# Optimization experiments

Measured on AMD Instinct MI355X. Metric: run time of the kernel, lower is better.

The kernel has to match this reference:

```python
import jax, jax.numpy as jnp
import numpy as np
from jax import lax

STRIDE = 16
RATIOS = (0.5, 1.0, 2.0)
SCALES = (128.0, 256.0, 512.0)


def _anchor_template():
    # template[i] = [stride/2, stride/2, w, h], i = ri*3 + si
    r = jnp.asarray(RATIOS, jnp.float32)[:, None]        # (3,1)
    s = jnp.asarray(SCALES, jnp.float32)[None, :]        # (1,3)
    sqrt_r = jnp.sqrt(r)
    w = (s / sqrt_r)                                     # (3,3)
    h = (s * sqrt_r)
    half = jnp.full_like(w, STRIDE / 2.0)
    return jnp.stack([half, half, w, h], axis=-1).reshape(9, 4)  # (9,4) xywh


def setup_inputs() -> dict:
    key = jax.random.key(0)
    ks = jax.random.split(key, 6)
    B, C, H, W = 8, 512, 50, 76
    feature_maps = jax.random.normal(ks[0], (B, C, H, W), jnp.float32)
    conv_w = jax.random.normal(ks[1], (512, 512, 3, 3), jnp.float32) * 0.01
    conv_b = jnp.zeros((512,), jnp.float32)
    cls_w = jax.random.normal(ks[2], (18, 512, 1, 1), jnp.float32) * 0.01
    cls_b = jnp.zeros((18,), jnp.float32)
    reg_w = jax.random.normal(ks[3], (36, 512, 1, 1), jnp.float32) * 0.01
    reg_b = jnp.zeros((36,), jnp.float32)
    # (width, height) per image; x is clamped to im_size[0], y to im_size[1]
    img_size = jnp.tile(jnp.array([[W * STRIDE, H * STRIDE]], jnp.int32), (B, 1))
    return {"feature_maps": feature_maps, "conv_w": conv_w, "conv_b": conv_b,
            "cls_w": cls_w, "cls_b": cls_b, "reg_w": reg_w, "reg_b": reg_b,
            "img_size": img_size}


def reference(feature_maps, conv_w, conv_b, cls_w, cls_b, reg_w, reg_b, img_size):
    B, C, H, W = feature_maps.shape
    # 3x3 conv, pad=1, stride=1 + ReLU
    f = lax.conv_general_dilated(feature_maps, conv_w, (1, 1), 'SAME',
                                 dimension_numbers=('NCHW', 'OIHW', 'NCHW'))
    f = jax.nn.relu(f + conv_b[None, :, None, None])
    # 1x1 heads, then NCHW -> BHWC (matches the two torch transposes)
    cls = jnp.einsum('bchw,oc->bhwo', f, cls_w.reshape(18, 512)) + cls_b
    reg = jnp.einsum('bchw,oc->bhwo', f, reg_w.reshape(36, 512)) + reg_b
    cls = cls.reshape(B, H, W, 9, 2)
    reg = reg.reshape(B, H, W, 9, 4)

    # Vectorized anchor generation (replaces nested hi/wi loops)
    tmpl = _anchor_template()                              # (9,4)
    sx = (jnp.arange(W, dtype=jnp.float32) * STRIDE)[None, :]   # (1,W)
    sy = (jnp.arange(H, dtype=jnp.float32) * STRIDE)[:, None]   # (H,1)
    zeros = jnp.zeros((H, W), jnp.float32)
    shift = jnp.stack([jnp.broadcast_to(sx, (H, W)),
                       jnp.broadcast_to(sy, (H, W)), zeros, zeros], axis=-1)  # (H,W,4)
    anchors = tmpl[None, None] + shift[:, :, None, :]      # (H,W,9,4)
    anchors = jnp.broadcast_to(anchors, (B, H, W, 9, 4)).reshape(B, -1, 4)

    cls = cls.reshape(B, -1, 2)
    reg = reg.reshape(B, -1, 4)

    # anchor2bbox: inverse of the target encoding in loss()
    axy, awh = anchors[..., :2], anchors[..., 2:]
    pxy = axy + reg[..., :2] * awh
    pwh = awh * jnp.exp(reg[..., 2:])

    # eval-mode clip to image bounds (vectorized over batch)
    im = img_size.astype(jnp.float32)[:, None, :]          # (B,1,2) = (w,h)
    x1y1 = pxy - pwh / 2
    x2y2 = x1y1 + pwh
    x1y1 = jnp.clip(x1y1, 0.0, im)
    x2y2 = jnp.clip(x2y2, 0.0, im)
    wh = x2y2 - x1y1
    cxy = x1y1 + wh / 2
    proposals = jnp.concatenate([cxy, wh], axis=-1)        # (B, H*W*9, 4)
    return (proposals, cls)
```

## Files before the change

### kernel.cpp

```cpp
#include <hip/hip_runtime.h>

typedef __attribute__((ext_vector_type(8))) __bf16 bf16x8;
typedef __attribute__((ext_vector_type(4))) float  f32x4;

#define GPTR(p)   (__attribute__((address_space(1))) void*)(p)
#define LDSPTR(p) (__attribute__((address_space(3))) void*)(p)
#define MFMA16 __builtin_amdgcn_mfma_f32_16x16x32_bf16
#define SB() __builtin_amdgcn_sched_barrier(0)

__device__ __forceinline__ unsigned short f2bf(float f) {
    union { float f; unsigned u; } v; v.f = f;
    unsigned r = v.u + 0x7FFF + ((v.u >> 16) & 1);
    return (unsigned short)(r >> 16);
}

#define MTOT   30400
#define MPAD   30464
#define KTOT   4608
#define NT     72

__global__ __launch_bounds__(256) void prep_all(
    const float* __restrict__ cw,
    const float* __restrict__ cls_w, const float* __restrict__ reg_w,
    const float* __restrict__ cls_b, const float* __restrict__ reg_b,
    const float* __restrict__ fm,
    unsigned short* __restrict__ Wt,
    unsigned short* __restrict__ W2, float* __restrict__ b2,
    unsigned short* __restrict__ P)
{
    __shared__ float t[32][65];
    int bid = blockIdx.x;
    if (bid < 9216) {
        int i = bid * 256 + threadIdx.x;
        int o = i / KTOT;
        int r = i - o * KTOT;
        int kk = r >> 9;
        int c  = r & 511;
        Wt[i] = f2bf(cw[(o * 512 + c) * 9 + kk]);
    } else if (bid < 9344) {
        int i = (bid - 9216) * 256 + threadIdx.x;
        int n = i >> 9, k = i & 511;
        float v = 0.f;
        if (n < 18) v = cls_w[n * 512 + k];
        else if (n < 54) v = reg_w[(n - 18) * 512 + k];
        W2[i] = f2bf(v);
        if (i < 64) {
            float bv = 0.f;
            if (i < 18) bv = cls_b[i];
            else if (i < 54) bv = reg_b[i - 18];
            b2[i] = bv;
        }
    } else if (bid < 9856) {
        int i = (bid - 9344) * 256 + threadIdx.x;
        int b   = i >> 14;
        int rem = i & 16383;
        int seg = rem >> 6;
        int c8  = (rem & 63) << 3;
        int y, x;
        if (seg < 78)       { y = 0;  x = seg; }
        else if (seg < 156) { y = 51; x = seg - 78; }
        else if (seg < 206) { y = seg - 155; x = 0; }
        else                { y = seg - 205; x = 77; }
        *(float4*)(P + ((b * 52 + y) * 78 + x) * 512 + c8) = make_float4(0.f, 0.f, 0.f, 0.f);
    } else {
        int bid2 = bid - 9856;
        const int tid = threadIdx.x;
        const int tx  = tid & 31;
        const int ty  = tid >> 5;
        const int xp  = bid2 % 24;
        const int tix = xp % 3;
        const int cix = xp / 3;
        const int y   = (bid2 / 24) % 50;
        const int b   = bid2 / 1200;
        const int x0  = tix * 32, c0 = cix * 64;

        const int x = x0 + tx;
        if (x < 76) {
#pragma unroll
            for (int i = 0; i < 8; ++i) {
                int cc = i * 8 + ty;
                t[tx][cc] = fm[((b * 512 + c0 + cc) * 50 + y) * 76 + x];
            }
        }
        __syncthreads();

        const int p = tid >> 6;
        const int c = tid & 63;
#pragma unroll
        for (int xi = 0; xi < 8; ++xi) {
            int xr = p * 8 + xi;
            int xw = x0 + xr;
            if (xw < 76)
                P[((b * 52 + y + 1) * 78 + (xw + 1)) * 512 + c0 + c] = f2bf(t[xr][c]);
        }
    }
}

__global__ __launch_bounds__(512, 2) void conv_gemm8(
    const unsigned short* __restrict__ P,
    const unsigned short* __restrict__ Wt,
    const float* __restrict__ bias,
    unsigned short* __restrict__ F)
{
    __shared__ __attribute__((aligned(1024))) unsigned char lds[131072];

    const int tid = threadIdx.x;
    const int l   = tid & 63;
    const int w   = tid >> 6;
    const int wr  = w >> 2;
    const int nc  = w & 3;
    const int hB  = nc >> 1;
    const int rB  = (nc & 1) * 4;

    const int orig = blockIdx.y * 119 + blockIdx.x;
    const int xcd = orig & 7, seq = orig >> 3;
    const int wg  = (xcd < 6 ? xcd * 30 : 180 + (xcd - 6) * 29) + seq;
    const int m0  = (wg % 119) * 256;
    const int n0  = (wg / 119) * 256;

    const int loff = (l & 15) * 64 + (((l >> 4) * 16) ^ ((l & 8) ? 32 : 0));
    const int kelS = ((l & 3) * 8) ^ ((l & 32) ? 16 : 0);

    int cbA[2][2], nbB[2][2];
#pragma unroll
    for (int h = 0; h < 2; ++h)
#pragma unroll
        for (int j = 0; j < 2; ++j) {
            const int s    = j * 8 + w;
            const int rowt = h * 128 + (s >> 1) * 16 + (l >> 2);
            int m = m0 + rowt; if (m >= MTOT) m = 0;
            int b = m / 3800; int r = m - b * 3800;
            int y = r / 76;   int x = r - y * 76;
            cbA[h][j] = ((b * 52 + y + 1) * 78 + (x + 1)) * 512 + (s & 1) * 32 + kelS;
            nbB[h][j] = (n0 + rowt) * KTOT + (s & 1) * 32 + kelS;
        }

    auto stA = [&](int t, int h, unsigned char* abase) {
        const int kk  = t >> 3;
        const int tap = ((kk / 3 - 1) * 78 + (kk % 3 - 1)) * 512 + (t & 7) * 64;
#pragma unroll
        for (int j = 0; j < 2; ++j)
            __builtin_amdgcn_global_load_lds(GPTR(P + cbA[h][j] + tap),
                LDSPTR(abase + h * 16384 + j * 8192 + w * 1024), 16, 0, 0);
    };
    auto stB = [&](int t, int h, unsigned char* bbase) {
#pragma unroll
        for (int j = 0; j < 2; ++j)
            __builtin_amdgcn_global_load_lds(GPTR(Wt + nbB[h][j] + t * 64),
                LDSPTR(bbase + h * 16384 + j * 8192 + w * 1024), 16, 0, 0);
    };

    f32x4 acc[8][4];
#pragma unroll
    for (int i = 0; i < 8; ++i)
#pragma unroll
        for (int j = 0; j < 4; ++j) acc[i][j] = (f32x4){0.f, 0.f, 0.f, 0.f};

#define RD(basep, subR, ks) (*(const bf16x8*)((basep) + (((subR) * 2 + (ks)) * 1024) + loff))

    {
        unsigned char* A0b = lds;
        unsigned char* B0b = lds + 32768;
        stB(0, 0, B0b); stB(0, 1, B0b); stA(0, 0, A0b); stA(0, 1, A0b);
        __syncthreads();
    }

    for (int g = 0; g < NT; ++g) {
        unsigned char* Ac = lds + (g & 1) * 65536;
        unsigned char* Bc = Ac + 32768;
        unsigned char* An = lds + (((g & 1) ^ 1)) * 65536;
        unsigned char* Bn = An + 32768;
        unsigned char* Ah = Ac + wr * 16384;
        unsigned char* Bh = Bc + hB * 16384;

        if (g + 1 < NT) {
            stB(g + 1, 0, Bn); stB(g + 1, 1, Bn);
            stA(g + 1, 0, An); stA(g + 1, 1, An);
        }
        SB();

#pragma unroll
        for (int ks = 0; ks < 2; ++ks) {
            bf16x8 a[8], b[4];
#pragma unroll
            for (int f = 0; f < 8; ++f) a[f] = RD(Ah, f, ks);
#pragma unroll
            for (int n = 0; n < 4; ++n) b[n] = RD(Bh, rB + n, ks);
#pragma unroll
            for (int n = 0; n < 4; ++n)
#pragma unroll
                for (int f = 0; f < 8; ++f)
                    acc[f][n] = MFMA16(a[f], b[n], acc[f][n], 0, 0, 0);
        }

        __syncthreads();
    }
#undef RD

#pragma unroll
    for (int ni = 0; ni < 4; ++ni) {
        const int col = n0 + nc * 64 + ni * 16 + (l & 15);
        const float bcol = bias[col];
#pragma unroll
        for (int mi = 0; mi < 8; ++mi) {
#pragma unroll
            for (int jj = 0; jj < 4; ++jj) {
                const int row = m0 + wr * 128 + mi * 16 + (l >> 4) * 4 + jj;
                if (row < MTOT)
                    F[row * 512 + col] = f2bf(fmaxf(acc[mi][ni][jj] + bcol, 0.f));
            }
        }
    }
}

__global__ __launch_bounds__(256) void head_decode(
    const unsigned short* __restrict__ F,
    const unsigned short* __restrict__ W2,
    const float* __restrict__ b2,
    const int* __restrict__ img,
    float* __restrict__ out)
{
    __shared__ float S[64][56];
    const int tid  = threadIdx.x;
    const int lane = tid & 63;
    const int wv   = tid >> 6;
    const int mblk = blockIdx.x * 64;
    int arow = mblk + wv * 16 + (lane & 15);
    if (arow >= MTOT) arow = MTOT - 1;

    f32x4 acc[4];
#pragma unroll
    for (int ni = 0; ni < 4; ++ni) acc[ni] = (f32x4){0.f, 0.f, 0.f, 0.f};

#pragma unroll 4
    for (int ks = 0; ks < 16; ++ks) {
        const int kloc = ks * 32 + (lane >> 4) * 8;
        bf16x8 a = *(const bf16x8*)(F + arow * 512 + kloc);
#pragma unroll
        for (int ni = 0; ni < 4; ++ni) {
            bf16x8 b = *(const bf16x8*)(W2 + (ni * 16 + (lane & 15)) * 512 + kloc);
            acc[ni] = MFMA16(a, b, acc[ni], 0, 0, 0);
        }
    }

#pragma unroll
    for (int ni = 0; ni < 4; ++ni) {
        int col = ni * 16 + (lane & 15);
        if (col < 54) {
            float bb = b2[col];
#pragma unroll
            for (int j = 0; j < 4; ++j)
                S[wv * 16 + (lane >> 4) * 4 + j][col] = acc[ni][j] + bb;
        }
    }
    __syncthreads();

    for (int it = tid; it < 576; it += 256) {
        int rowl = it / 9;
        int a    = it - rowl * 9;
        int m = mblk + rowl;
        if (m >= MTOT) continue;
        int b   = m / 3800;
        int rem = m - b * 3800;
        int y = rem / 76;
        int x = rem - y * 76;

        int ri = a / 3, si = a - ri * 3;
        float sqr = (ri == 0) ? 0.70710678118654752f : ((ri == 1) ? 1.f : 1.41421356237309515f);
        float scale = (float)(128 << si);
        float wa = scale / sqr;
        float ha = scale * sqr;
        float ax = (float)x * 16.f + 8.f;
        float ay = (float)y * 16.f + 8.f;

        float r0 = S[rowl][18 + a * 4 + 0];
        float r1 = S[rowl][18 + a * 4 + 1];
        float r2 = S[rowl][18 + a * 4 + 2];
        float r3 = S[rowl][18 + a * 4 + 3];

        float px = ax + r0 * wa;
        float py = ay + r1 * ha;
        float pw = wa * expf(r2);
        float ph = ha * expf(r3);

        float x1 = px - 0.5f * pw, y1 = py - 0.5f * ph;
        float x2 = x1 + pw,        y2 = y1 + ph;
        float imx = (float)img[2 * b], imy = (float)img[2 * b + 1];
        x1 = fminf(fmaxf(x1, 0.f), imx); x2 = fminf(fmaxf(x2, 0.f), imx);
        y1 = fminf(fmaxf(y1, 0.f), imy); y2 = fminf(fmaxf(y2, 0.f), imy);
        float ww = x2 - x1, hh = y2 - y1;
        float cx = x1 + 0.5f * ww, cy = y1 + 0.5f * hh;

        int pidx = b * 34200 + rem * 9 + a;
        ((float4*)out)[pidx] = make_float4(cx, cy, ww, hh);
        float* oc = out + 1094400 + pidx * 2;
        oc[0] = S[rowl][a * 2 + 0];
        oc[1] = S[rowl][a * 2 + 1];
    }
}

extern "C" void kernel_launch(void* const* d_in, const int* in_sizes, int n_in,
                              void* d_out, int out_size, void* d_ws, size_t ws_size,
                              hipStream_t stream) {
    const float* fm     = (const float*)d_in[0];
    const float* conv_w = (const float*)d_in[1];
    const float* conv_b = (const float*)d_in[2];
    const float* cls_w  = (const float*)d_in[3];
    const float* cls_b  = (const float*)d_in[4];
    const float* reg_w  = (const float*)d_in[5];
    const float* reg_b  = (const float*)d_in[6];
    const int*   img    = (const int*)d_in[7];
    float* out = (float*)d_out;

    char* ws = (char*)d_ws;
    unsigned short* P  = (unsigned short*)(ws);
    unsigned short* Wt = (unsigned short*)(ws + 33226752);
    unsigned short* F  = (unsigned short*)(ws + 37945344);
    unsigned short* W2 = (unsigned short*)(ws + 69140480);
    float*          b2 = (float*)(ws + 69206016);

    prep_all<<<19456, 256, 0, stream>>>(conv_w, cls_w, reg_w, cls_b, reg_b, fm,
                                        Wt, W2, b2, P);
    conv_gemm8<<<dim3(119, 2), 512, 0, stream>>>(P, Wt, conv_b, F);
    head_decode<<<475, 256, 0, stream>>>(F, W2, b2, img, out);
}
```

Before: 189.9 us.

## Load conv weight fragments directly from global into registers, halving LDS

The B operand (weights) is no longer staged through LDS with global_load_lds. Each wave reads its own MFMA B fragments straight from global memory into registers every k-step, and LDS shrinks to a 64KB double buffer for A only. The aim is to cut LDS traffic and footprint. In exchange, every wave re-reads the weights from global or L2 with no cross-wave sharing, and these loads are issued right before the MFMAs with no prefetch, so their latency may be exposed.

```diff
diff --git a/kernel.cpp b/kernel.cpp
--- a/kernel.cpp
+++ b/kernel.cpp
@@ -102,15 +102,13 @@
     const float* __restrict__ bias,
     unsigned short* __restrict__ F)
 {
-    __shared__ __attribute__((aligned(1024))) unsigned char lds[131072];
+    __shared__ __attribute__((aligned(1024))) unsigned char lds[65536];
 
     const int tid = threadIdx.x;
     const int l   = tid & 63;
     const int w   = tid >> 6;
     const int wr  = w >> 2;
     const int nc  = w & 3;
-    const int hB  = nc >> 1;
-    const int rB  = (nc & 1) * 4;
 
     const int orig = blockIdx.y * 119 + blockIdx.x;
     const int xcd = orig & 7, seq = orig >> 3;
@@ -121,7 +119,7 @@
     const int loff = (l & 15) * 64 + (((l >> 4) * 16) ^ ((l & 8) ? 32 : 0));
     const int kelS = ((l & 3) * 8) ^ ((l & 32) ? 16 : 0);
 
-    int cbA[2][2], nbB[2][2];
+    int cbA[2][2];
 #pragma unroll
     for (int h = 0; h < 2; ++h)
 #pragma unroll
@@ -132,8 +130,12 @@
             int b = m / 3800; int r = m - b * 3800;
             int y = r / 76;   int x = r - y * 76;
             cbA[h][j] = ((b * 52 + y + 1) * 78 + (x + 1)) * 512 + (s & 1) * 32 + kelS;
-            nbB[h][j] = (n0 + rowt) * KTOT + (s & 1) * 32 + kelS;
-        }
+        }
+
+    int bB[4];
+#pragma unroll
+    for (int ni = 0; ni < 4; ++ni)
+        bB[ni] = (n0 + nc * 64 + ni * 16 + (l & 15)) * KTOT + ((l >> 4) * 8);
 
     auto stA = [&](int t, int h, unsigned char* abase) {
         const int kk  = t >> 3;
@@ -143,12 +145,6 @@
             __builtin_amdgcn_global_load_lds(GPTR(P + cbA[h][j] + tap),
                 LDSPTR(abase + h * 16384 + j * 8192 + w * 1024), 16, 0, 0);
     };
-    auto stB = [&](int t, int h, unsigned char* bbase) {
-#pragma unroll
-        for (int j = 0; j < 2; ++j)
-            __builtin_amdgcn_global_load_lds(GPTR(Wt + nbB[h][j] + t * 64),
-                LDSPTR(bbase + h * 16384 + j * 8192 + w * 1024), 16, 0, 0);
-    };
 
     f32x4 acc[8][4];
 #pragma unroll
@@ -158,39 +154,34 @@
 
 #define RD(basep, subR, ks) (*(const bf16x8*)((basep) + (((subR) * 2 + (ks)) * 1024) + loff))
 
-    {
-        unsigned char* A0b = lds;
-        unsigned char* B0b = lds + 32768;
-        stB(0, 0, B0b); stB(0, 1, B0b); stA(0, 0, A0b); stA(0, 1, A0b);
-        __syncthreads();
-    }
+    stA(0, 0, lds); stA(0, 1, lds);
+    __syncthreads();
 
     for (int g = 0; g < NT; ++g) {
-        unsigned char* Ac = lds + (g & 1) * 65536;
-        unsigned char* Bc = Ac + 32768;
-        unsigned char* An = lds + (((g & 1) ^ 1)) * 65536;
-        unsigned char* Bn = An + 32768;
+        unsigned char* Ac = lds + (g & 1) * 32768;
+        unsigned char* An = lds + (((g & 1) ^ 1)) * 32768;
         unsigned char* Ah = Ac + wr * 16384;
-        unsigned char* Bh = Bc + hB * 16384;
-
-        if (g + 1 < NT) {
-            stB(g + 1, 0, Bn); stB(g + 1, 1, Bn);
-            stA(g + 1, 0, An); stA(g + 1, 1, An);
+
+        if (g + 1 < NT) { stA(g + 1, 0, An); stA(g + 1, 1, An); }
+
+        bf16x8 b0[4], b1[4];
+#pragma unroll
+        for (int ni = 0; ni < 4; ++ni) {
+            b0[ni] = *(const bf16x8*)(Wt + bB[ni] + g * 64);
+            b1[ni] = *(const bf16x8*)(Wt + bB[ni] + g * 64 + 32);
         }
         SB();
 
 #pragma unroll
         for (int ks = 0; ks < 2; ++ks) {
-            bf16x8 a[8], b[4];
+            bf16x8 a[8];
 #pragma unroll
             for (int f = 0; f < 8; ++f) a[f] = RD(Ah, f, ks);
 #pragma unroll
-            for (int n = 0; n < 4; ++n) b[n] = RD(Bh, rB + n, ks);
-#pragma unroll
             for (int n = 0; n < 4; ++n)
 #pragma unroll
                 for (int f = 0; f < 8; ++f)
-                    acc[f][n] = MFMA16(a[f], b[n], acc[f][n], 0, 0, 0);
+                    acc[f][n] = MFMA16(a[f], (ks ? b1 : b0)[n], acc[f][n], 0, 0, 0);
         }
 
         __syncthreads();
```

New measurement: 277.0 us. 1.46x slower.

## Triple-buffer A tiles and use partial vmcnt waits in conv GEMM

Applied to the files above, without the earlier changes.

The LDS buffer grows to hold three A (im2col activation) stages and two B (weight) stages. A tiles are now prefetched two K-steps ahead and B tiles one step ahead. The full __syncthreads drain at the end of each step becomes an s_waitcnt vmcnt(4) plus a raw barrier, so the newest A prefetch can stay in flight across the barrier. The aim is to hide the latency of the scattered activation gather. The cost is 160KB of LDS (the whole CU) and hand-tuned wait counts that must match the number of loads issued per stage.

```diff
diff --git a/kernel.cpp b/kernel.cpp
--- a/kernel.cpp
+++ b/kernel.cpp
@@ -102,7 +102,7 @@
     const float* __restrict__ bias,
     unsigned short* __restrict__ F)
 {
-    __shared__ __attribute__((aligned(1024))) unsigned char lds[131072];
+    __shared__ __attribute__((aligned(1024))) unsigned char lds[163840];
 
     const int tid = threadIdx.x;
     const int l   = tid & 63;
@@ -135,19 +135,23 @@
             nbB[h][j] = (n0 + rowt) * KTOT + (s & 1) * 32 + kelS;
         }
 
-    auto stA = [&](int t, int h, unsigned char* abase) {
+    auto stA = [&](int t, unsigned char* abase) {
         const int kk  = t >> 3;
         const int tap = ((kk / 3 - 1) * 78 + (kk % 3 - 1)) * 512 + (t & 7) * 64;
 #pragma unroll
-        for (int j = 0; j < 2; ++j)
-            __builtin_amdgcn_global_load_lds(GPTR(P + cbA[h][j] + tap),
-                LDSPTR(abase + h * 16384 + j * 8192 + w * 1024), 16, 0, 0);
+        for (int h = 0; h < 2; ++h)
+#pragma unroll
+            for (int j = 0; j < 2; ++j)
+                __builtin_amdgcn_global_load_lds(GPTR(P + cbA[h][j] + tap),
+                    LDSPTR(abase + h * 16384 + j * 8192 + w * 1024), 16, 0, 0);
     };
-    auto stB = [&](int t, int h, unsigned char* bbase) {
-#pragma unroll
-        for (int j = 0; j < 2; ++j)
-            __builtin_amdgcn_global_load_lds(GPTR(Wt + nbB[h][j] + t * 64),
-                LDSPTR(bbase + h * 16384 + j * 8192 + w * 1024), 16, 0, 0);
+    auto stB = [&](int t, unsigned char* bbase) {
+#pragma unroll
+        for (int h = 0; h < 2; ++h)
+#pragma unroll
+            for (int j = 0; j < 2; ++j)
+                __builtin_amdgcn_global_load_lds(GPTR(Wt + nbB[h][j] + t * 64),
+                    LDSPTR(bbase + h * 16384 + j * 8192 + w * 1024), 16, 0, 0);
     };
 
     f32x4 acc[8][4];
@@ -157,26 +161,23 @@
         for (int j = 0; j < 4; ++j) acc[i][j] = (f32x4){0.f, 0.f, 0.f, 0.f};
 
 #define RD(basep, subR, ks) (*(const bf16x8*)((basep) + (((subR) * 2 + (ks)) * 1024) + loff))
-
-    {
-        unsigned char* A0b = lds;
-        unsigned char* B0b = lds + 32768;
-        stB(0, 0, B0b); stB(0, 1, B0b); stA(0, 0, A0b); stA(0, 1, A0b);
-        __syncthreads();
-    }
+#define ABUF(t) (lds + ((t) % 3) * 32768)
+#define BBUF(t) (lds + 98304 + ((t) & 1) * 32768)
+
+    stB(0, BBUF(0));
+    stA(0, ABUF(0));
+    stA(1, ABUF(1));
+    SB();
+    asm volatile("s_waitcnt vmcnt(4)" ::: "memory");
+    __builtin_amdgcn_s_barrier();
+    SB();
 
     for (int g = 0; g < NT; ++g) {
-        unsigned char* Ac = lds + (g & 1) * 65536;
-        unsigned char* Bc = Ac + 32768;
-        unsigned char* An = lds + (((g & 1) ^ 1)) * 65536;
-        unsigned char* Bn = An + 32768;
-        unsigned char* Ah = Ac + wr * 16384;
-        unsigned char* Bh = Bc + hB * 16384;
-
-        if (g + 1 < NT) {
-            stB(g + 1, 0, Bn); stB(g + 1, 1, Bn);
-            stA(g + 1, 0, An); stA(g + 1, 1, An);
-        }
+        unsigned char* Ah = ABUF(g) + wr * 16384;
+        unsigned char* Bh = BBUF(g) + hB * 16384;
+
+        if (g + 1 < NT) stB(g + 1, BBUF(g + 1));
+        if (g + 2 < NT) stA(g + 2, ABUF(g + 2));
         SB();
 
 #pragma unroll
@@ -193,8 +194,14 @@
                     acc[f][n] = MFMA16(a[f], b[n], acc[f][n], 0, 0, 0);
         }
 
-        __syncthreads();
-    }
+        SB();
+        if (g + 2 < NT)       asm volatile("s_waitcnt vmcnt(4)" ::: "memory");
+        else if (g + 1 < NT)  asm volatile("s_waitcnt vmcnt(0)" ::: "memory");
+        __builtin_amdgcn_s_barrier();
+        SB();
+    }
+#undef ABUF
+#undef BBUF
 #undef RD
 
 #pragma unroll
```

After: 192.5 us. About the same (+1.4%).
